# Optimization experiments

Measured on AMD Instinct MI355X. Metric: run time of the kernel, lower is better.

The kernel has to match this reference:

```python
import jax, jax.numpy as jnp
import numpy as np

B, T, D = 2, 2048, 1024
H = 16
DH = D // H
SCALE = DH ** -0.5


def setup_inputs() -> dict:
    key = jax.random.key(0)
    ks = jax.random.split(key, 10)
    s = lambda fan_in: 1.0 / np.sqrt(fan_in)
    # weights stored (in, out) so y = x @ W + b (torch Linear transposed)
    return {
        "x": jax.random.normal(ks[0], (B, T, D), dtype=jnp.float32),
        "Wqkv0": jax.random.uniform(ks[1], (D, 3 * D), jnp.float32, -s(D), s(D)),
        "bqkv0": jax.random.uniform(ks[2], (3 * D,), jnp.float32, -s(D), s(D)),
        "Wqkv1": jax.random.uniform(ks[3], (D, 3 * D), jnp.float32, -s(D), s(D)),
        "bqkv1": jax.random.uniform(ks[4], (3 * D,), jnp.float32, -s(D), s(D)),
        "Wg": jax.random.uniform(ks[5], (2 * D, D), jnp.float32, -s(2 * D), s(2 * D)),
        "bg": jax.random.uniform(ks[6], (D,), jnp.float32, -s(2 * D), s(2 * D)),
        "Wo": jax.random.uniform(ks[7], (D, D), jnp.float32, -s(D), s(D)),
        "bo": jax.random.uniform(ks[8], (D,), jnp.float32, -s(D), s(D)),
    }


def _attend(x, Wqkv, bqkv):
    # x: [B,T,D] -> qkv: [B,T,3,H,DH]
    qkv = (x @ Wqkv + bqkv).reshape(B, T, 3, H, DH)
    q, k, v = qkv[:, :, 0], qkv[:, :, 1], qkv[:, :, 2]  # [B,T,H,DH]
    scores = jnp.einsum("bqhd,bkhd->bhqk", q, k) * SCALE
    causal = jnp.tril(jnp.ones((T, T), dtype=bool))
    scores = jnp.where(causal, scores, jnp.finfo(scores.dtype).min)
    attn = jax.nn.softmax(scores, axis=-1)  # dropout is identity in eval mode
    out = jnp.einsum("bhqk,bkhd->bqhd", attn, v)
    return out.reshape(B, T, D)


def reference(x, Wqkv0, bqkv0, Wqkv1, bqkv1, Wg, bg, Wo, bo):
    pred = _attend(x, Wqkv0, bqkv0)
    output = pred
    cumulative = pred
    # n_rounds = 2 -> one correction round
    residual = x - cumulative
    correction = _attend(residual, Wqkv1, bqkv1)
    gate = jax.nn.sigmoid(jnp.concatenate([cumulative, correction], axis=-1) @ Wg + bg)
    gated = gate * correction
    output = output + gated
    return output @ Wo + bo
```

## Files before the change

### kernel.cpp

```cpp
#include <hip/hip_runtime.h>
#include <hip/hip_bf16.h>


typedef __bf16 bf16x8 __attribute__((ext_vector_type(8)));
typedef float f32x4 __attribute__((ext_vector_type(4)));

__device__ __forceinline__ unsigned short f2bf(float f) {
  union { __hip_bfloat16 h; unsigned short u; } cv;
  cv.h = __float2bfloat16(f);
  return cv.u;
}

#define GLD16(gp, lp) __builtin_amdgcn_global_load_lds(                      \
    (const __attribute__((address_space(1))) void*)(gp),                     \
    (__attribute__((address_space(3))) void*)(lp), 16, 0, 0)

__global__ __launch_bounds__(256) void transpose_cast(
    const float* __restrict__ in, __hip_bfloat16* __restrict__ out, int R, int C) {
  __shared__ float t[32][33];
  int bx = blockIdx.x * 32, by = blockIdx.y * 32;
  int tx = threadIdx.x, ty = threadIdx.y;
#pragma unroll
  for (int i = 0; i < 32; i += 8)
    t[ty + i][tx] = in[(size_t)(by + ty + i) * C + bx + tx];
  __syncthreads();
#pragma unroll
  for (int i = 0; i < 32; i += 8)
    out[(size_t)(bx + ty + i) * R + by + tx] = __float2bfloat16(t[tx][ty + i]);
}

__global__ __launch_bounds__(256) void cast_f32_bf16(
    const float* __restrict__ in, __hip_bfloat16* __restrict__ out) {
  size_t e = ((size_t)blockIdx.x * blockDim.x + threadIdx.x) * 4;
  float4 v = *(const float4*)(in + e);
  ushort4 o;
  o.x = f2bf(v.x); o.y = f2bf(v.y); o.z = f2bf(v.z); o.w = f2bf(v.w);
  *(ushort4*)((unsigned short*)out + e) = o;
}

__global__ __launch_bounds__(256) void resid_cast(
    const float* __restrict__ x, const __hip_bfloat16* __restrict__ catb,
    __hip_bfloat16* __restrict__ residb) {
  size_t e = ((size_t)blockIdx.x * blockDim.x + threadIdx.x) * 4;
  float4 xv = *(const float4*)(x + e);
  size_t row = e >> 10, col = e & 1023;
  ushort4 pb = *(const ushort4*)((const unsigned short*)catb + row * 2048 + col);
  union { unsigned int u; float f; } c0, c1, c2, c3;
  c0.u = (unsigned int)pb.x << 16; c1.u = (unsigned int)pb.y << 16;
  c2.u = (unsigned int)pb.z << 16; c3.u = (unsigned int)pb.w << 16;
  ushort4 rb;
  rb.x = f2bf(xv.x - c0.f); rb.y = f2bf(xv.y - c1.f);
  rb.z = f2bf(xv.z - c2.f); rb.w = f2bf(xv.w - c3.f);
  *(ushort4*)((unsigned short*)residb + e) = rb;
}

template <int EPI>
__global__ __launch_bounds__(256) void gemm_bf16(
    const __hip_bfloat16* __restrict__ A, const __hip_bfloat16* __restrict__ Bt,
    const float* __restrict__ bias, void* __restrict__ outp,
    const __hip_bfloat16* __restrict__ aux0, const __hip_bfloat16* __restrict__ aux1,
    int M, int N, int K) {
  __shared__ __hip_bfloat16 As[2][128 * 32];
  __shared__ __hip_bfloat16 Bs[2][128 * 32];
  const int tid = threadIdx.x;
  const int lane = tid & 63, wid = tid >> 6;
  const int wr = wid >> 1, wc = wid & 1;
  const int lr = lane & 15, lk = (lane >> 4) * 8;
  const size_t brow = (size_t)blockIdx.y * 128, bcol = (size_t)blockIdx.x * 128;
  f32x4 acc[4][4] = {};
#pragma unroll
  for (int r = 0; r < 2; ++r) {
    int c = tid + r * 256;
    GLD16(A + (brow + (size_t)(c >> 2)) * K + (c & 3) * 8, As[0] + c * 8);
    GLD16(Bt + (bcol + (size_t)(c >> 2)) * K + (c & 3) * 8, Bs[0] + c * 8);
  }
  __syncthreads();
  int cur = 0;
  for (int k0 = 0; k0 < K; k0 += 32) {
    const int nxt = cur ^ 1;
    if (k0 + 32 < K) {
#pragma unroll
      for (int r = 0; r < 2; ++r) {
        int c = tid + r * 256;
        GLD16(A + (brow + (size_t)(c >> 2)) * K + k0 + 32 + (c & 3) * 8,
              As[nxt] + c * 8);
        GLD16(Bt + (bcol + (size_t)(c >> 2)) * K + k0 + 32 + (c & 3) * 8,
              Bs[nxt] + c * 8);
      }
    }
    bf16x8 a[4], b[4];
#pragma unroll
    for (int m = 0; m < 4; ++m)
      a[m] = *(const bf16x8*)(As[cur] + (wr * 64 + m * 16 + lr) * 32 + lk);
#pragma unroll
    for (int n = 0; n < 4; ++n)
      b[n] = *(const bf16x8*)(Bs[cur] + (wc * 64 + n * 16 + lr) * 32 + lk);
#pragma unroll
    for (int m = 0; m < 4; ++m)
#pragma unroll
      for (int n = 0; n < 4; ++n)
        acc[m][n] = __builtin_amdgcn_mfma_f32_16x16x32_bf16(a[m], b[n], acc[m][n], 0, 0, 0);
    __syncthreads();
    cur = nxt;
  }
  const int r0 = (lane >> 4) * 4, cn = lane & 15;
#pragma unroll
  for (int m = 0; m < 4; ++m)
#pragma unroll
    for (int n = 0; n < 4; ++n) {
      size_t col = bcol + wc * 64 + n * 16 + cn;
      float bv = bias[col];
#pragma unroll
      for (int j = 0; j < 4; ++j) {
        size_t row = brow + wr * 64 + m * 16 + r0 + j;
        float v = acc[m][n][j] + bv;
        if constexpr (EPI == 1) {
          float g = 1.0f / (1.0f + __expf(-v));
          float a0 = __bfloat162float(aux0[row * 2048 + col]);
          float a1 = __bfloat162float(aux1[row * 2048 + col]);
          ((__hip_bfloat16*)outp)[row * N + col] = __float2bfloat16(g * a0 + a1);
        } else if constexpr (EPI == 2) {
          ((float*)outp)[row * N + col] = v;
        } else {
          ((__hip_bfloat16*)outp)[row * N + col] = __float2bfloat16(v);
        }
      }
    }
}

__global__ __launch_bounds__(256) void attn_kernel(
    const __hip_bfloat16* __restrict__ qkv,
    __hip_bfloat16* __restrict__ outb, int ob_off) {
  const int b = blockIdx.z, h = blockIdx.y, qtp = blockIdx.x;
  const int qlo = qtp, qhi = 31 - qtp;
  const int q0lo = qlo * 64, q0hi = qhi * 64;
  __shared__ __hip_bfloat16 ks[2][64 * 64];
  __shared__ __hip_bfloat16 vts[2][64 * 64];
  __shared__ __hip_bfloat16 qps[8192];
  const int tid = threadIdx.x, lane = tid & 63, w = tid >> 6;
  const int lr = lane & 15, lg = lane >> 4;
  const int sw = lr & 7;
  const size_t rs = 3072;
  const __hip_bfloat16* qbh = qkv + ((size_t)b * 2048 + q0hi) * rs + h * 64;
  const __hip_bfloat16* qbl = qkv + ((size_t)b * 2048 + q0lo) * rs + h * 64;
  const __hip_bfloat16* kb = qkv + (size_t)b * 2048 * rs + 1024 + h * 64;
  const __hip_bfloat16* vb = qkv + (size_t)b * 2048 * rs + 2048 + h * 64;

  const int vrow2 = tid >> 3, vseg = tid & 7;
  float4 vr0, vr1;
#pragma unroll
  for (int r = 0; r < 2; ++r) {
    int c = tid + r * 256, row = c >> 3, p = c & 7;
    GLD16(qbh + (size_t)row * rs + (p ^ (row & 7)) * 8, qps + c * 8);
    GLD16(qbl + (size_t)row * rs + (p ^ (row & 7)) * 8, qps + 4096 + c * 8);
    GLD16(kb + (size_t)row * rs + (p ^ (row & 7)) * 8, ks[0] + c * 8);
  }
  vr0 = *(const float4*)(vb + (size_t)(2 * vrow2) * rs + vseg * 8);
  vr1 = *(const float4*)(vb + (size_t)(2 * vrow2 + 1) * rs + vseg * 8);
  __syncthreads();
  const int qrow = w * 16 + lr;
  const bf16x8 qh0 = *(const bf16x8*)(qps + qrow * 64 + ((lg) ^ (qrow & 7)) * 8);
  const bf16x8 qh1 = *(const bf16x8*)(qps + qrow * 64 + ((4 + lg) ^ (qrow & 7)) * 8);
  const bf16x8 ql0 = *(const bf16x8*)(qps + 4096 + qrow * 64 + ((lg) ^ (qrow & 7)) * 8);
  const bf16x8 ql1 = *(const bf16x8*)(qps + 4096 + qrow * 64 + ((4 + lg) ^ (qrow & 7)) * 8);
  {
    const unsigned short* u0 = (const unsigned short*)&vr0;
    const unsigned short* u1 = (const unsigned short*)&vr1;
#pragma unroll
    for (int i = 0; i < 8; ++i) {
      const int dh = vseg * 8 + i;
      const int phys = (vrow2 >> 2) ^ (dh & 7) ^ ((dh >> 3) & 7);
      unsigned int pk = (unsigned int)u0[i] | ((unsigned int)u1[i] << 16);
      *(unsigned int*)(vts[0] + dh * 64 + phys * 8 + 2 * (vrow2 & 3)) = pk;
    }
  }
  __syncthreads();

  __hip_bfloat16* psh = qps + w * 1024;
  __hip_bfloat16* psl = qps + 4096 + w * 1024;
  float m_hi = -1e30f, l_hi = 0.f, m_lo = -1e30f, l_lo = 0.f;
  f32x4 o_hi[4] = {}, o_lo[4] = {};
  int cur = 0;

  auto process = [&](const bf16x8& qa0, const bf16x8& qa1, bool diag,
                     float& m_run, float& l_run, f32x4* o, __hip_bfloat16* psw) {
    f32x4 s4[4] = {};
    __builtin_amdgcn_s_setprio(1);
#pragma unroll
    for (int n = 0; n < 4; ++n) {
      const int kr = n * 16 + lr;
      bf16x8 k0f = *(const bf16x8*)(ks[cur] + kr * 64 + ((lg) ^ sw) * 8);
      bf16x8 k1f = *(const bf16x8*)(ks[cur] + kr * 64 + ((4 + lg) ^ sw) * 8);
      s4[n] = __builtin_amdgcn_mfma_f32_16x16x32_bf16(k0f, qa0, s4[n], 0, 0, 0);
      s4[n] = __builtin_amdgcn_mfma_f32_16x16x32_bf16(k1f, qa1, s4[n], 0, 0, 0);
    }
    __builtin_amdgcn_s_setprio(0);
    float p[4][4];
    float mloc = -1e30f;
#pragma unroll
    for (int n = 0; n < 4; ++n)
#pragma unroll
      for (int j = 0; j < 4; ++j) {
        float v = s4[n][j] * 0.125f;
        if (diag && (n * 16 + lg * 4 + j) > (w * 16 + lr)) v = -1e30f;
        p[n][j] = v;
        mloc = fmaxf(mloc, v);
      }
    mloc = fmaxf(mloc, __shfl_xor(mloc, 16));
    mloc = fmaxf(mloc, __shfl_xor(mloc, 32));
    const float mn = fmaxf(m_run, mloc);
    const float sc = __expf(m_run - mn);
    m_run = mn;
    float ls = 0.f;
#pragma unroll
    for (int n = 0; n < 4; ++n)
#pragma unroll
      for (int j = 0; j < 4; ++j) { p[n][j] = __expf(p[n][j] - mn); ls += p[n][j]; }
    ls += __shfl_xor(ls, 16);
    ls += __shfl_xor(ls, 32);
    l_run = l_run * sc + ls;
    float scb[4];
#pragma unroll
    for (int j = 0; j < 4; ++j) scb[j] = __shfl(sc, lg * 4 + j);
#pragma unroll
    for (int n = 0; n < 4; ++n)
#pragma unroll
      for (int j = 0; j < 4; ++j) o[n][j] *= scb[j];
#pragma unroll
    for (int n = 0; n < 4; ++n)
#pragma unroll
      for (int j = 0; j < 4; ++j)
        psw[lr * 64 + ((n * 2 + (lg >> 1)) ^ sw) * 8 + (lg & 1) * 4 + j] =
            __float2bfloat16(p[n][j]);
    bf16x8 pa0 = *(const bf16x8*)(&psw[lr * 64 + ((lg) ^ sw) * 8]);
    bf16x8 pa1 = *(const bf16x8*)(&psw[lr * 64 + ((4 + lg) ^ sw) * 8]);
    __builtin_amdgcn_s_setprio(1);
#pragma unroll
    for (int n = 0; n < 4; ++n) {
      const int vdh = n * 16 + lr;
      const int swv = (vdh & 7) ^ ((vdh >> 3) & 7);
      bf16x8 v0f = *(const bf16x8*)(vts[cur] + vdh * 64 + ((lg) ^ swv) * 8);
      bf16x8 v1f = *(const bf16x8*)(vts[cur] + vdh * 64 + ((4 + lg) ^ swv) * 8);
      o[n] = __builtin_amdgcn_mfma_f32_16x16x32_bf16(pa0, v0f, o[n], 0, 0, 0);
      o[n] = __builtin_amdgcn_mfma_f32_16x16x32_bf16(pa1, v1f, o[n], 0, 0, 0);
    }
    __builtin_amdgcn_s_setprio(0);
  };

  for (int kvt = 0; kvt <= qhi; ++kvt) {
    const int nxt = cur ^ 1;
    const bool pf = (kvt < qhi);
    if (pf) {
      const int kv1 = (kvt + 1) * 64;
#pragma unroll
      for (int r = 0; r < 2; ++r) {
        int c = tid + r * 256, row = c >> 3, p = c & 7;
        GLD16(kb + (size_t)(kv1 + row) * rs + (p ^ (row & 7)) * 8, ks[nxt] + c * 8);
      }
      vr0 = *(const float4*)(vb + (size_t)(kv1 + 2 * vrow2) * rs + vseg * 8);
      vr1 = *(const float4*)(vb + (size_t)(kv1 + 2 * vrow2 + 1) * rs + vseg * 8);
    }
    process(qh0, qh1, kvt == qhi, m_hi, l_hi, o_hi, psh);
    if (kvt <= qlo) process(ql0, ql1, kvt == qlo, m_lo, l_lo, o_lo, psl);
    if (pf) {
      const unsigned short* u0 = (const unsigned short*)&vr0;
      const unsigned short* u1 = (const unsigned short*)&vr1;
#pragma unroll
      for (int i = 0; i < 8; ++i) {
        const int dh = vseg * 8 + i;
        const int phys = (vrow2 >> 2) ^ (dh & 7) ^ ((dh >> 3) & 7);
        unsigned int pk = (unsigned int)u0[i] | ((unsigned int)u1[i] << 16);
        *(unsigned int*)(vts[nxt] + dh * 64 + phys * 8 + 2 * (vrow2 & 3)) = pk;
      }
    }
    __syncthreads();
    cur = nxt;
  }
  const float linv_h = 1.0f / l_hi, linv_l = 1.0f / l_lo;
#pragma unroll
  for (int j = 0; j < 4; ++j) {
    const float lih = __shfl(linv_h, lg * 4 + j);
    const float lil = __shfl(linv_l, lg * 4 + j);
    size_t rowh = (size_t)b * 2048 + q0hi + w * 16 + lg * 4 + j;
    size_t rowl = (size_t)b * 2048 + q0lo + w * 16 + lg * 4 + j;
#pragma unroll
    for (int n = 0; n < 4; ++n) {
      outb[rowh * 2048 + ob_off + h * 64 + n * 16 + lr] = __float2bfloat16(o_hi[n][j] * lih);
      outb[rowl * 2048 + ob_off + h * 64 + n * 16 + lr] = __float2bfloat16(o_lo[n][j] * lil);
    }
  }
}

extern "C" void kernel_launch(void* const* d_in, const int* in_sizes, int n_in,
                              void* d_out, int out_size, void* d_ws, size_t ws_size,
                              hipStream_t stream) {
  const float* x     = (const float*)d_in[0];
  const float* Wqkv0 = (const float*)d_in[1];
  const float* bqkv0 = (const float*)d_in[2];
  const float* Wqkv1 = (const float*)d_in[3];
  const float* bqkv1 = (const float*)d_in[4];
  const float* Wg    = (const float*)d_in[5];
  const float* bg    = (const float*)d_in[6];
  const float* Wo    = (const float*)d_in[7];
  const float* bo    = (const float*)d_in[8];
  float* out = (float*)d_out;

  char* ws = (char*)d_ws;
  __hip_bfloat16* xb   = (__hip_bfloat16*)(ws);
  __hip_bfloat16* qkv  = (__hip_bfloat16*)(ws + 8388608);
  __hip_bfloat16* catb = (__hip_bfloat16*)(ws + 67108864);
  __hip_bfloat16* Wt0  = (__hip_bfloat16*)(ws + 83886080);
  __hip_bfloat16* Wt1  = (__hip_bfloat16*)(ws + 90177536);
  __hip_bfloat16* Wgt  = (__hip_bfloat16*)(ws + 96468992);
  __hip_bfloat16* Wot  = (__hip_bfloat16*)(ws + 100663296);

  dim3 tb(32, 8);
  transpose_cast<<<dim3(3072 / 32, 1024 / 32), tb, 0, stream>>>(Wqkv0, Wt0, 1024, 3072);
  transpose_cast<<<dim3(3072 / 32, 1024 / 32), tb, 0, stream>>>(Wqkv1, Wt1, 1024, 3072);
  transpose_cast<<<dim3(1024 / 32, 2048 / 32), tb, 0, stream>>>(Wg, Wgt, 2048, 1024);
  transpose_cast<<<dim3(1024 / 32, 1024 / 32), tb, 0, stream>>>(Wo, Wot, 1024, 1024);
  cast_f32_bf16<<<4096, 256, 0, stream>>>(x, xb);

  gemm_bf16<0><<<dim3(24, 32), 256, 0, stream>>>(xb, Wt0, bqkv0, (void*)qkv,
                                                 nullptr, nullptr, 4096, 3072, 1024);
  attn_kernel<<<dim3(16, 16, 2), 256, 0, stream>>>(qkv, catb, 0);
  resid_cast<<<4096, 256, 0, stream>>>(x, catb, xb);
  gemm_bf16<0><<<dim3(24, 32), 256, 0, stream>>>(xb, Wt1, bqkv1, (void*)qkv,
                                                 nullptr, nullptr, 4096, 3072, 1024);
  attn_kernel<<<dim3(16, 16, 2), 256, 0, stream>>>(qkv, catb, 1024);
  gemm_bf16<1><<<dim3(8, 32), 256, 0, stream>>>(catb, Wgt, bg, (void*)xb,
                                                catb + 1024, catb, 4096, 1024, 2048);
  gemm_bf16<2><<<dim3(8, 32), 256, 0, stream>>>(xb, Wot, bo, (void*)out,
                                                nullptr, nullptr, 4096, 1024, 1024);
}
```

Before: 297.4 us.

## Batch prep kernels, fuse residual into attention, add lazy softmax rescale

Merges the four weight transpose-casts and the input cast into one launch that selects its job from the block index. Computes the residual x - pred in the first attention kernel's epilogue, which removes the separate resid_cast kernel and its re-read of the attention output. Adds a lazy online-softmax rescale: the running max and the output accumulators are only updated when some row's new max exceeds the old by more than 8. This skips shuffles and multiplies in the common case, at the cost of exponentials up to e^8 that fp32 can hold.

```diff
diff --git a/kernel.cpp b/kernel.cpp
--- a/kernel.cpp
+++ b/kernel.cpp
@@ -15,11 +15,30 @@
     (const __attribute__((address_space(1))) void*)(gp),                     \
     (__attribute__((address_space(3))) void*)(lp), 16, 0, 0)
 
-__global__ __launch_bounds__(256) void transpose_cast(
-    const float* __restrict__ in, __hip_bfloat16* __restrict__ out, int R, int C) {
+__global__ __launch_bounds__(256) void prep_batch(
+    const float* __restrict__ W0, __hip_bfloat16* __restrict__ Wt0,
+    const float* __restrict__ W1, __hip_bfloat16* __restrict__ Wt1,
+    const float* __restrict__ Wg, __hip_bfloat16* __restrict__ Wgt,
+    const float* __restrict__ Wo, __hip_bfloat16* __restrict__ Wot,
+    const float* __restrict__ x, __hip_bfloat16* __restrict__ xb) {
+  const int bid = blockIdx.x;
+  if (bid >= 9216) {
+    size_t e = (((size_t)(bid - 9216)) * 256 + threadIdx.x) * 4;
+    float4 v = *(const float4*)(x + e);
+    ushort4 o;
+    o.x = f2bf(v.x); o.y = f2bf(v.y); o.z = f2bf(v.z); o.w = f2bf(v.w);
+    *(ushort4*)((unsigned short*)xb + e) = o;
+    return;
+  }
+  const float* in; __hip_bfloat16* out; int R, C, base;
+  if (bid < 3072)      { in = W0; out = Wt0; R = 1024; C = 3072; base = 0; }
+  else if (bid < 6144) { in = W1; out = Wt1; R = 1024; C = 3072; base = 3072; }
+  else if (bid < 8192) { in = Wg; out = Wgt; R = 2048; C = 1024; base = 6144; }
+  else                 { in = Wo; out = Wot; R = 1024; C = 1024; base = 8192; }
+  const int local = bid - base, nbx = C / 32;
+  const int bx = (local % nbx) * 32, by = (local / nbx) * 32;
+  const int tx = threadIdx.x & 31, ty = threadIdx.x >> 5;
   __shared__ float t[32][33];
-  int bx = blockIdx.x * 32, by = blockIdx.y * 32;
-  int tx = threadIdx.x, ty = threadIdx.y;
 #pragma unroll
   for (int i = 0; i < 32; i += 8)
     t[ty + i][tx] = in[(size_t)(by + ty + i) * C + bx + tx];
@@ -27,31 +46,6 @@
 #pragma unroll
   for (int i = 0; i < 32; i += 8)
     out[(size_t)(bx + ty + i) * R + by + tx] = __float2bfloat16(t[tx][ty + i]);
-}
-
-__global__ __launch_bounds__(256) void cast_f32_bf16(
-    const float* __restrict__ in, __hip_bfloat16* __restrict__ out) {
-  size_t e = ((size_t)blockIdx.x * blockDim.x + threadIdx.x) * 4;
-  float4 v = *(const float4*)(in + e);
-  ushort4 o;
-  o.x = f2bf(v.x); o.y = f2bf(v.y); o.z = f2bf(v.z); o.w = f2bf(v.w);
-  *(ushort4*)((unsigned short*)out + e) = o;
-}
-
-__global__ __launch_bounds__(256) void resid_cast(
-    const float* __restrict__ x, const __hip_bfloat16* __restrict__ catb,
-    __hip_bfloat16* __restrict__ residb) {
-  size_t e = ((size_t)blockIdx.x * blockDim.x + threadIdx.x) * 4;
-  float4 xv = *(const float4*)(x + e);
-  size_t row = e >> 10, col = e & 1023;
-  ushort4 pb = *(const ushort4*)((const unsigned short*)catb + row * 2048 + col);
-  union { unsigned int u; float f; } c0, c1, c2, c3;
-  c0.u = (unsigned int)pb.x << 16; c1.u = (unsigned int)pb.y << 16;
-  c2.u = (unsigned int)pb.z << 16; c3.u = (unsigned int)pb.w << 16;
-  ushort4 rb;
-  rb.x = f2bf(xv.x - c0.f); rb.y = f2bf(xv.y - c1.f);
-  rb.z = f2bf(xv.z - c2.f); rb.w = f2bf(xv.w - c3.f);
-  *(ushort4*)((unsigned short*)residb + e) = rb;
 }
 
 template <int EPI>
@@ -130,7 +124,8 @@
 
 __global__ __launch_bounds__(256) void attn_kernel(
     const __hip_bfloat16* __restrict__ qkv,
-    __hip_bfloat16* __restrict__ outb, int ob_off) {
+    __hip_bfloat16* __restrict__ outb, int ob_off,
+    const float* __restrict__ xg, __hip_bfloat16* __restrict__ residb) {
   const int b = blockIdx.z, h = blockIdx.y, qtp = blockIdx.x;
   const int qlo = qtp, qhi = 31 - qtp;
   const int q0lo = qlo * 64, q0hi = qhi * 64;
@@ -208,24 +203,27 @@
       }
     mloc = fmaxf(mloc, __shfl_xor(mloc, 16));
     mloc = fmaxf(mloc, __shfl_xor(mloc, 32));
-    const float mn = fmaxf(m_run, mloc);
-    const float sc = __expf(m_run - mn);
-    m_run = mn;
+    if (!__all(mloc - m_run <= 8.0f)) {
+      const float mn = fmaxf(m_run, mloc);
+      const float sc = __expf(m_run - mn);
+      m_run = mn;
+      l_run *= sc;
+      float scb[4];
+#pragma unroll
+      for (int j = 0; j < 4; ++j) scb[j] = __shfl(sc, lg * 4 + j);
+#pragma unroll
+      for (int n = 0; n < 4; ++n)
+#pragma unroll
+        for (int j = 0; j < 4; ++j) o[n][j] *= scb[j];
+    }
     float ls = 0.f;
 #pragma unroll
     for (int n = 0; n < 4; ++n)
 #pragma unroll
-      for (int j = 0; j < 4; ++j) { p[n][j] = __expf(p[n][j] - mn); ls += p[n][j]; }
+      for (int j = 0; j < 4; ++j) { p[n][j] = __expf(p[n][j] - m_run); ls += p[n][j]; }
     ls += __shfl_xor(ls, 16);
     ls += __shfl_xor(ls, 32);
-    l_run = l_run * sc + ls;
-    float scb[4];
-#pragma unroll
-    for (int j = 0; j < 4; ++j) scb[j] = __shfl(sc, lg * 4 + j);
-#pragma unroll
-    for (int n = 0; n < 4; ++n)
-#pragma unroll
-      for (int j = 0; j < 4; ++j) o[n][j] *= scb[j];
+    l_run += ls;
 #pragma unroll
     for (int n = 0; n < 4; ++n)
 #pragma unroll
@@ -285,8 +283,14 @@
     size_t rowl = (size_t)b * 2048 + q0lo + w * 16 + lg * 4 + j;
 #pragma unroll
     for (int n = 0; n < 4; ++n) {
-      outb[rowh * 2048 + ob_off + h * 64 + n * 16 + lr] = __float2bfloat16(o_hi[n][j] * lih);
-      outb[rowl * 2048 + ob_off + h * 64 + n * 16 + lr] = __float2bfloat16(o_lo[n][j] * lil);
+      float vh = o_hi[n][j] * lih, vl = o_lo[n][j] * lil;
+      const int col = h * 64 + n * 16 + lr;
+      outb[rowh * 2048 + ob_off + col] = __float2bfloat16(vh);
+      outb[rowl * 2048 + ob_off + col] = __float2bfloat16(vl);
+      if (ob_off == 0) {
+        residb[rowh * 1024 + col] = __float2bfloat16(xg[rowh * 1024 + col] - vh);
+        residb[rowl * 1024 + col] = __float2bfloat16(xg[rowl * 1024 + col] - vl);
+      }
     }
   }
 }
@@ -314,20 +318,15 @@
   __hip_bfloat16* Wgt  = (__hip_bfloat16*)(ws + 96468992);
   __hip_bfloat16* Wot  = (__hip_bfloat16*)(ws + 100663296);
 
-  dim3 tb(32, 8);
-  transpose_cast<<<dim3(3072 / 32, 1024 / 32), tb, 0, stream>>>(Wqkv0, Wt0, 1024, 3072);
-  transpose_cast<<<dim3(3072 / 32, 1024 / 32), tb, 0, stream>>>(Wqkv1, Wt1, 1024, 3072);
-  transpose_cast<<<dim3(1024 / 32, 2048 / 32), tb, 0, stream>>>(Wg, Wgt, 2048, 1024);
-  transpose_cast<<<dim3(1024 / 32, 1024 / 32), tb, 0, stream>>>(Wo, Wot, 1024, 1024);
-  cast_f32_bf16<<<4096, 256, 0, stream>>>(x, xb);
+  prep_batch<<<13312, 256, 0, stream>>>(Wqkv0, Wt0, Wqkv1, Wt1, Wg, Wgt,
+                                        Wo, Wot, x, xb);
 
   gemm_bf16<0><<<dim3(24, 32), 256, 0, stream>>>(xb, Wt0, bqkv0, (void*)qkv,
                                                  nullptr, nullptr, 4096, 3072, 1024);
-  attn_kernel<<<dim3(16, 16, 2), 256, 0, stream>>>(qkv, catb, 0);
-  resid_cast<<<4096, 256, 0, stream>>>(x, catb, xb);
+  attn_kernel<<<dim3(16, 16, 2), 256, 0, stream>>>(qkv, catb, 0, x, xb);
   gemm_bf16<0><<<dim3(24, 32), 256, 0, stream>>>(xb, Wt1, bqkv1, (void*)qkv,
                                                  nullptr, nullptr, 4096, 3072, 1024);
-  attn_kernel<<<dim3(16, 16, 2), 256, 0, stream>>>(qkv, catb, 1024);
+  attn_kernel<<<dim3(16, 16, 2), 256, 0, stream>>>(qkv, catb, 1024, nullptr, nullptr);
   gemm_bf16<1><<<dim3(8, 32), 256, 0, stream>>>(catb, Wgt, bg, (void*)xb,
                                                 catb + 1024, catb, 4096, 1024, 2048);
   gemm_bf16<2><<<dim3(8, 32), 256, 0, stream>>>(xb, Wot, bo, (void*)out,
```

Result: faster. 287.0 us (-3.5%).
